# Performance work log

Hardware: AMD Instinct MI355X
Metric: run time of the kernel (lower is better)

The kernel has to match this reference:

```python
import jax, jax.numpy as jnp
import numpy as np

HIDDEN = 1024
HEADS = 16
HEAD_DIM = HIDDEN // HEADS


def setup_inputs() -> dict:
    key = jax.random.key(0)
    ks = jax.random.split(key, 11)
    B, S = 2, 2048
    s = 1.0 / np.sqrt(HIDDEN)
    return {
        "query": jax.random.normal(ks[0], (B, S, HIDDEN), jnp.float32),
        "key": jax.random.normal(ks[1], (B, S, HIDDEN), jnp.float32),
        "value": jax.random.normal(ks[2], (B, S, HIDDEN), jnp.float32),
        "Wq": jax.random.uniform(ks[3], (HIDDEN, HIDDEN), jnp.float32, -s, s),
        "bq": jax.random.uniform(ks[4], (HIDDEN,), jnp.float32, -s, s),
        "Wk": jax.random.uniform(ks[5], (HIDDEN, HIDDEN), jnp.float32, -s, s),
        "bk": jax.random.uniform(ks[6], (HIDDEN,), jnp.float32, -s, s),
        "Wv": jax.random.uniform(ks[7], (HIDDEN, HIDDEN), jnp.float32, -s, s),
        "bv": jax.random.uniform(ks[8], (HIDDEN,), jnp.float32, -s, s),
        "Wo": jax.random.uniform(ks[9], (HIDDEN, HIDDEN), jnp.float32, -s, s),
        "bo": jax.random.uniform(ks[10], (HIDDEN,), jnp.float32, -s, s),
    }


def reference(query, key, value, Wq, bq, Wk, bk, Wv, bv, Wo, bo):
    B, Sq, _ = query.shape
    Sk = key.shape[1]
    # projections (torch Linear: x @ W^T + b)
    Q = (query @ Wq.T + bq).reshape(B, Sq, HEADS, HEAD_DIM).transpose(0, 2, 1, 3)
    K = (key @ Wk.T + bk).reshape(B, Sk, HEADS, HEAD_DIM).transpose(0, 2, 1, 3)
    V = (value @ Wv.T + bv).reshape(B, Sk, HEADS, HEAD_DIM).transpose(0, 2, 1, 3)
    scale = jnp.sqrt(jnp.float32(HEAD_DIM))
    scores = jnp.einsum("bhqd,bhkd->bhqk", Q, K) / scale  # [B,H,Sq,Sk]
    # causal mask (is_causal=True, Sq>1)
    causal = jnp.tril(jnp.ones((Sq, Sk), dtype=bool))
    scores = jnp.where(causal[None, None], scores, -jnp.inf)
    attn = jax.nn.softmax(scores, axis=-1)
    out = jnp.einsum("bhqk,bhkd->bhqd", attn, V)
    out = out.transpose(0, 2, 1, 3).reshape(B, Sq, HIDDEN)
    return out @ Wo.T + bo
```

## Files before the change

### kernel.cpp

```cpp
#include <hip/hip_runtime.h>
#include <hip/hip_bf16.h>


typedef __attribute__((ext_vector_type(4))) float f32x4;
typedef __attribute__((ext_vector_type(8))) short bf16x8;
typedef unsigned short u16;

#define SEQ   2048
#define NH    16
#define HD    64
#define HID   1024
#define CEXP  0.1803368801f
#define MEG   1048576u

#define BAR()  __builtin_amdgcn_s_barrier()
#define SCHED0() __builtin_amdgcn_sched_barrier(0)

static __device__ __forceinline__ u16 f2bf(float f) {
  union { __hip_bfloat16 h; u16 u; } c;
  c.h = __float2bfloat16(f);
  return c.u;
}

static __device__ __forceinline__ int swz(int row, int col8) {
  return col8 ^ ((row & 7) << 3);
}

static __device__ __forceinline__ void gll16(const void* g, void* l) {
  __builtin_amdgcn_global_load_lds(
      (const __attribute__((address_space(1))) void*)g,
      (__attribute__((address_space(3))) void*)l, 16, 0, 0);
}

__global__ __launch_bounds__(256) void cvt_kernel(
    const float* __restrict__ Wq, const float* __restrict__ Wk,
    const float* __restrict__ Wv, const float* __restrict__ Wo,
    const float* __restrict__ q, const float* __restrict__ k,
    const float* __restrict__ v,
    u16* __restrict__ wsout, u16* __restrict__ dob) {
  const int y = blockIdx.y;
  const int c = y & 3;
  const float* src;
  u16* dst;
  if (y < 4) {
    src = (y == 0) ? Wq : (y == 1) ? Wk : (y == 2) ? Wv : Wo;
    dst = wsout + (size_t)y * MEG;
  } else if (y < 8) {
    src = q + (size_t)c * MEG;
    dst = wsout + 4u * MEG + (size_t)c * MEG;
  } else if (y < 12) {
    src = k + (size_t)c * MEG;
    dst = dob + (size_t)c * MEG;
  } else {
    src = v + (size_t)c * MEG;
    dst = dob + 4u * MEG + (size_t)c * MEG;
  }
  int i = (blockIdx.x * 256 + threadIdx.x) * 4;
  float4 f = *(const float4*)(src + i);
  ushort4 o;
  o.x = f2bf(f.x); o.y = f2bf(f.y); o.z = f2bf(f.z); o.w = f2bf(f.w);
  *(ushort4*)(dst + i) = o;
}

__global__ __launch_bounds__(256) void proj_kernel(
    const u16* __restrict__ Xq, const u16* __restrict__ Xk,
    const u16* __restrict__ Xv, const u16* __restrict__ Wc,
    const float* __restrict__ bq, const float* __restrict__ bk,
    const float* __restrict__ bvp,
    u16* __restrict__ Qo, u16* __restrict__ Ko, u16* __restrict__ Vto) {
  __shared__ u16 As[2][128 * 64];
  __shared__ u16 Bs[2][128 * 64];

  const int tid  = threadIdx.x;
  const int lane = tid & 63;
  const int wid  = tid >> 6;
  const int wm   = wid >> 1, wn = wid & 1;
  const int l15  = lane & 15;
  const int lhi  = lane >> 4;
  const int z    = blockIdx.z;
  const int bm   = blockIdx.x * 128;
  const int bn   = blockIdx.y * 128;

  const u16* X = (z == 0) ? Xq : (z == 1) ? Xk : Xv;
  const u16* W = Wc + (size_t)z * (HID * HID);
  const float* bias = (z == 0) ? bq : (z == 1) ? bk : bvp;

  f32x4 acc[4][4];
#pragma unroll
  for (int i = 0; i < 4; i++)
#pragma unroll
    for (int j = 0; j < 4; j++) acc[i][j] = (f32x4){0.f, 0.f, 0.f, 0.f};

  const int lrow  = lane >> 3;
  const int gcol8 = lane & 7;

#define PROJ_STAGE(buf, k0)                                                       \
  {                                                                               \
    _Pragma("unroll")                                                             \
    for (int c = 0; c < 4; c++) {                                                 \
      const int row  = c * 32 + wid * 8 + lrow;                                   \
      const int scol = (gcol8 ^ (row & 7)) * 8;      \
      gll16(X + (size_t)(bm + row) * HID + (k0) + scol,                           \
            (char*)&As[buf][0] + c * 4096 + wid * 1024);                          \
      gll16(W + (size_t)(bn + row) * HID + (k0) + scol,                           \
            (char*)&Bs[buf][0] + c * 4096 + wid * 1024);                          \
    }                                                                             \
  }

  PROJ_STAGE(0, 0);
  for (int t = 0; t < 16; t++) {
    BAR();
    if (t < 15) {
      PROJ_STAGE((t + 1) & 1, (t + 1) * 64);
      asm volatile("s_waitcnt vmcnt(8)" ::: "memory");
    } else {
      asm volatile("s_waitcnt vmcnt(0)" ::: "memory");
    }
    BAR();
    SCHED0();
    const u16* A = &As[t & 1][0];
    const u16* B = &Bs[t & 1][0];
#pragma unroll
    for (int ks = 0; ks < 2; ks++) {
      bf16x8 af[4], bfm[4];
#pragma unroll
      for (int i = 0; i < 4; i++) {
        const int row = wm * 64 + i * 16 + l15;
        af[i] = *(const bf16x8*)&A[row * 64 + swz(row, ks * 32 + lhi * 8)];
      }
#pragma unroll
      for (int j = 0; j < 4; j++) {
        const int row = wn * 64 + j * 16 + l15;
        bfm[j] = *(const bf16x8*)&B[row * 64 + swz(row, ks * 32 + lhi * 8)];
      }
#pragma unroll
      for (int i = 0; i < 4; i++)
#pragma unroll
        for (int j = 0; j < 4; j++)
          acc[i][j] = __builtin_amdgcn_mfma_f32_16x16x32_bf16(af[i], bfm[j], acc[i][j], 0, 0, 0);
    }
  }
#undef PROJ_STAGE

  const int bb = bm >> 11;
#pragma unroll
  for (int j = 0; j < 4; j++) {
    const int n = bn + wn * 64 + j * 16 + l15;
    const float bv_ = bias[n];
    const int h = n >> 6, d = n & 63;
    if (z == 2) {
#pragma unroll
      for (int i = 0; i < 4; i++) {
        const int s0 = (bm + wm * 64 + i * 16 + lhi * 4) & 2047;
        ushort4 t;
        t.x = f2bf(acc[i][j][0] + bv_);
        t.y = f2bf(acc[i][j][1] + bv_);
        t.z = f2bf(acc[i][j][2] + bv_);
        t.w = f2bf(acc[i][j][3] + bv_);
        *(ushort4*)&Vto[((size_t)(bb * NH + h) * HD + d) * SEQ + s0] = t;
      }
    } else {
      u16* O = z ? Ko : Qo;
#pragma unroll
      for (int i = 0; i < 4; i++)
#pragma unroll
        for (int r = 0; r < 4; r++) {
          const int m = bm + wm * 64 + i * 16 + lhi * 4 + r;
          const int s = m & 2047;
          O[(((size_t)(bb * NH + h) * SEQ + s) << 6) + d] = f2bf(acc[i][j][r] + bv_);
        }
    }
  }
}

__global__ __launch_bounds__(512) void attn_kernel(
    const u16* __restrict__ Q, const u16* __restrict__ K,
    const u16* __restrict__ Vt, u16* __restrict__ Aout) {
  __shared__ __align__(16) char pool[51200];

  const int tid  = threadIdx.x;
  const int lane = tid & 63;
  const int wid  = tid >> 6;
  const int rw   = wid & 3;
  const int g    = wid >> 2;
  const int l15  = lane & 15;
  const int lhi  = lane >> 4;

  const int flat = blockIdx.x;
  const int slot = flat >> 3;
  const int bh   = (flat & 7) * 4 + (slot & 3);
  const int qt   = 31 - (slot >> 2);
  const int b    = bh >> 4, h = bh & 15;
  const size_t base = (size_t)bh * SEQ * HD;

  u16* Ksh = (u16*)(pool + g * 8192);
  u16* Vsh = (u16*)(pool + 16384 + g * 8192);
  u16* Psh = (u16*)(pool + 32768 + wid * 2304);

  const int qrow = qt * 64 + rw * 16 + l15;
  bf16x8 aq[2];
  aq[0] = *(const bf16x8*)&Q[base + (size_t)qrow * HD + lhi * 8];
  aq[1] = *(const bf16x8*)&Q[base + (size_t)qrow * HD + 32 + lhi * 8];

  f32x4 o[4];
#pragma unroll
  for (int n = 0; n < 4; n++) o[n] = (f32x4){0.f, 0.f, 0.f, 0.f};
  float m_s = -1e30f, l_s = 0.f;

  const int gt   = tid & 255;
  const int srow = gt >> 2;
  const int sd   = (gt & 3) * 16;

  bf16x8 pk0, pk1, pv0, pv1;

#define ATTN_LOAD(kt_)                                                            \
  {                                                                               \
    const u16* kp = K + base + (size_t)((kt_) * 64 + srow) * HD + sd;             \
    pk0 = *(const bf16x8*)kp;                                                     \
    pk1 = *(const bf16x8*)(kp + 8);                                               \
    const u16* vp = Vt + base + (size_t)srow * SEQ + (kt_) * 64 + sd;             \
    pv0 = *(const bf16x8*)vp;                                                     \
    pv1 = *(const bf16x8*)(vp + 8);                                               \
  }

  if (g <= qt) ATTN_LOAD(g);

  const int nsteps = qt / 2 + 1;
  for (int it = 0; it < nsteps; ++it) {
    const int kt = 2 * it + g;
    const bool act = (kt <= qt);
    BAR();
    if (act) {
      *(bf16x8*)&Ksh[srow * 64 + swz(srow, sd)]     = pk0;
      *(bf16x8*)&Ksh[srow * 64 + swz(srow, sd + 8)] = pk1;
      *(bf16x8*)&Vsh[srow * 64 + swz(srow, sd)]     = pv0;
      *(bf16x8*)&Vsh[srow * 64 + swz(srow, sd + 8)] = pv1;
    }
    const int ktn = kt + 2;
    if (ktn <= qt) ATTN_LOAD(ktn);
    asm volatile("s_waitcnt lgkmcnt(0)" ::: "memory");
    BAR();
    SCHED0();
    if (act) {
      f32x4 sc[4];
      __builtin_amdgcn_s_setprio(1);
#pragma unroll
      for (int n = 0; n < 4; n++) {
        sc[n] = (f32x4){0.f, 0.f, 0.f, 0.f};
#pragma unroll
        for (int ks = 0; ks < 2; ks++) {
          const int krow = n * 16 + l15;
          bf16x8 bk = *(const bf16x8*)&Ksh[krow * 64 + swz(krow, ks * 32 + lhi * 8)];
          sc[n] = __builtin_amdgcn_mfma_f32_16x16x32_bf16(bk, aq[ks], sc[n], 0, 0, 0);
        }
      }
      __builtin_amdgcn_s_setprio(0);
      if (kt == qt) {
#pragma unroll
        for (int n = 0; n < 4; n++)
#pragma unroll
          for (int r = 0; r < 4; r++)
            if (kt * 64 + n * 16 + lhi * 4 + r > qrow) sc[n][r] = -1e30f;
      }
      float mx = -1e30f;
#pragma unroll
      for (int n = 0; n < 4; n++)
        mx = fmaxf(mx, fmaxf(fmaxf(sc[n][0], sc[n][1]), fmaxf(sc[n][2], sc[n][3])));
      mx = fmaxf(mx, __shfl_xor(mx, 16, 64));
      mx = fmaxf(mx, __shfl_xor(mx, 32, 64));
      if (__any(mx > m_s + 64.0f)) {
        const float mnew = fmaxf(m_s, mx);
        const float fac = __builtin_amdgcn_exp2f((m_s - mnew) * CEXP);
        l_s *= fac;
        m_s = mnew;
        float facr[4];
#pragma unroll
        for (int r = 0; r < 4; r++) facr[r] = __shfl(fac, lhi * 4 + r, 64);
#pragma unroll
        for (int n = 0; n < 4; n++) {
          o[n][0] *= facr[0]; o[n][1] *= facr[1];
          o[n][2] *= facr[2]; o[n][3] *= facr[3];
        }
      }
      const float nmc = -m_s * CEXP;
      float ps = 0.f;
      u16 pb[4][4];
#pragma unroll
      for (int n = 0; n < 4; n++)
#pragma unroll
        for (int r = 0; r < 4; r++) {
          const float e = __builtin_amdgcn_exp2f(fmaf(sc[n][r], CEXP, nmc));
          ps += e;
          pb[n][r] = f2bf(e);
        }
      ps += __shfl_xor(ps, 16, 64);
      ps += __shfl_xor(ps, 32, 64);
      l_s += ps;
#pragma unroll
      for (int n = 0; n < 4; n++) {
        ushort4 t; t.x = pb[n][0]; t.y = pb[n][1]; t.z = pb[n][2]; t.w = pb[n][3];
        *(ushort4*)&Psh[l15 * 72 + n * 16 + lhi * 4] = t;
      }
      bf16x8 ap0 = *(const bf16x8*)&Psh[l15 * 72 + lhi * 8];
      bf16x8 ap1 = *(const bf16x8*)&Psh[l15 * 72 + 32 + lhi * 8];
      __builtin_amdgcn_s_setprio(1);
#pragma unroll
      for (int n = 0; n < 4; n++) {
        const int vrow = n * 16 + l15;
        bf16x8 bv0 = *(const bf16x8*)&Vsh[vrow * 64 + swz(vrow, lhi * 8)];
        bf16x8 bv1 = *(const bf16x8*)&Vsh[vrow * 64 + swz(vrow, 32 + lhi * 8)];
        o[n] = __builtin_amdgcn_mfma_f32_16x16x32_bf16(ap0, bv0, o[n], 0, 0, 0);
        o[n] = __builtin_amdgcn_mfma_f32_16x16x32_bf16(ap1, bv1, o[n], 0, 0, 0);
      }
      __builtin_amdgcn_s_setprio(0);
    }
  }
#undef ATTN_LOAD

  __syncthreads();
  float m_o[4], l_o[4];
#pragma unroll
  for (int r = 0; r < 4; r++) {
    m_o[r] = __shfl(m_s, lhi * 4 + r, 64);
    l_o[r] = __shfl(l_s, lhi * 4 + r, 64);
  }

  f32x4* comb = (f32x4*)pool;
  const int ci = (rw * 64 + lane) * 6;
  if (g == 0) {
#pragma unroll
    for (int n = 0; n < 4; n++) comb[ci + n] = o[n];
    comb[ci + 4] = (f32x4){m_o[0], m_o[1], m_o[2], m_o[3]};
    comb[ci + 5] = (f32x4){l_o[0], l_o[1], l_o[2], l_o[3]};
  }
  __syncthreads();
  if (g == 1) {
    f32x4 m0 = comb[ci + 4];
    f32x4 l0 = comb[ci + 5];
    float a0[4], a1[4], inv[4];
#pragma unroll
    for (int r = 0; r < 4; r++) {
      const float m = fmaxf(m0[r], m_o[r]);
      a0[r] = __builtin_amdgcn_exp2f((m0[r] - m) * CEXP);
      a1[r] = __builtin_amdgcn_exp2f((m_o[r] - m) * CEXP);
      inv[r] = 1.0f / (l0[r] * a0[r] + l_o[r] * a1[r]);
    }
#pragma unroll
    for (int n = 0; n < 4; n++) {
      f32x4 o0 = comb[ci + n];
#pragma unroll
      for (int r = 0; r < 4; r++) {
        const int rowg = qt * 64 + rw * 16 + lhi * 4 + r;
        const float val = (o0[r] * a0[r] + o[n][r] * a1[r]) * inv[r];
        Aout[(((size_t)(b * SEQ + rowg)) << 10) + h * 64 + n * 16 + l15] = f2bf(val);
      }
    }
  }
}

__global__ __launch_bounds__(256) void oproj_kernel(
    const u16* __restrict__ X, const u16* __restrict__ W,
    const float* __restrict__ bias, float* __restrict__ Out) {
  __shared__ u16 As[2][128 * 64];
  __shared__ u16 Bs[2][64 * 64];

  const int tid  = threadIdx.x;
  const int lane = tid & 63;
  const int wid  = tid >> 6;
  const int wm   = wid >> 1, wn = wid & 1;
  const int l15  = lane & 15;
  const int lhi  = lane >> 4;
  const int bm   = blockIdx.x * 128;
  const int bn   = blockIdx.y * 64;

  f32x4 acc[4][2];
#pragma unroll
  for (int i = 0; i < 4; i++)
#pragma unroll
    for (int j = 0; j < 2; j++) acc[i][j] = (f32x4){0.f, 0.f, 0.f, 0.f};

  const int lrow  = lane >> 3;
  const int gcol8 = lane & 7;

#define OPROJ_STAGE(buf, k0)                                                      \
  {                                                                               \
    _Pragma("unroll")                                                             \
    for (int c = 0; c < 4; c++) {                                                 \
      const int row  = c * 32 + wid * 8 + lrow;                                   \
      const int scol = (gcol8 ^ (row & 7)) * 8;                                   \
      gll16(X + (size_t)(bm + row) * HID + (k0) + scol,                           \
            (char*)&As[buf][0] + c * 4096 + wid * 1024);                          \
      if (c < 2)                                                                  \
        gll16(W + (size_t)(bn + row) * HID + (k0) + scol,                         \
              (char*)&Bs[buf][0] + c * 4096 + wid * 1024);                        \
    }                                                                             \
  }

  OPROJ_STAGE(0, 0);
  for (int t = 0; t < 16; t++) {
    BAR();
    if (t < 15) {
      OPROJ_STAGE((t + 1) & 1, (t + 1) * 64);
      asm volatile("s_waitcnt vmcnt(6)" ::: "memory");
    } else {
      asm volatile("s_waitcnt vmcnt(0)" ::: "memory");
    }
    BAR();
    SCHED0();
    const u16* A = &As[t & 1][0];
    const u16* B = &Bs[t & 1][0];
#pragma unroll
    for (int ks = 0; ks < 2; ks++) {
      bf16x8 af[4], bfm[2];
#pragma unroll
      for (int i = 0; i < 4; i++) {
        const int row = wm * 64 + i * 16 + l15;
        af[i] = *(const bf16x8*)&A[row * 64 + swz(row, ks * 32 + lhi * 8)];
      }
#pragma unroll
      for (int j = 0; j < 2; j++) {
        const int row = wn * 32 + j * 16 + l15;
        bfm[j] = *(const bf16x8*)&B[row * 64 + swz(row, ks * 32 + lhi * 8)];
      }
#pragma unroll
      for (int i = 0; i < 4; i++)
#pragma unroll
        for (int j = 0; j < 2; j++)
          acc[i][j] = __builtin_amdgcn_mfma_f32_16x16x32_bf16(af[i], bfm[j], acc[i][j], 0, 0, 0);
    }
  }
#undef OPROJ_STAGE

#pragma unroll
  for (int j = 0; j < 2; j++) {
    const int n = bn + wn * 32 + j * 16 + l15;
    const float bv_ = bias[n];
#pragma unroll
    for (int i = 0; i < 4; i++)
#pragma unroll
      for (int r = 0; r < 4; r++) {
        const int m = bm + wm * 64 + i * 16 + lhi * 4 + r;
        Out[(size_t)m * HID + n] = acc[i][j][r] + bv_;
      }
  }
}

extern "C" void kernel_launch(void* const* d_in, const int* in_sizes, int n_in,
                              void* d_out, int out_size, void* d_ws, size_t ws_size,
                              hipStream_t stream) {
  const float* q  = (const float*)d_in[0];
  const float* k  = (const float*)d_in[1];
  const float* v  = (const float*)d_in[2];
  const float* Wq = (const float*)d_in[3];
  const float* bq = (const float*)d_in[4];
  const float* Wk = (const float*)d_in[5];
  const float* bk = (const float*)d_in[6];
  const float* Wv = (const float*)d_in[7];
  const float* bv = (const float*)d_in[8];
  const float* Wo = (const float*)d_in[9];
  const float* bo = (const float*)d_in[10];

  u16* ws   = (u16*)d_ws;
  u16* wqkv = ws;
  u16* wob  = ws + 3u * MEG;
  u16* qb   = ws + 4u * MEG;
  u16* Qb   = ws + 8u * MEG;
  u16* Kb   = ws + 12u * MEG;
  u16* Vtb  = ws + 16u * MEG;
  u16* Ab   = qb;
  u16* kbf  = (u16*)d_out;
  u16* vbf  = (u16*)d_out + 4u * MEG;

  cvt_kernel<<<dim3(1024, 16), 256, 0, stream>>>(Wq, Wk, Wv, Wo, q, k, v, ws, kbf);

  proj_kernel<<<dim3(32, 8, 3), 256, 0, stream>>>(qb, kbf, vbf, wqkv, bq, bk, bv,
                                                  Qb, Kb, Vtb);

  attn_kernel<<<dim3(1024), 512, 0, stream>>>(Qb, Kb, Vtb, Ab);

  oproj_kernel<<<dim3(32, 16), 256, 0, stream>>>(Ab, wob, bo, (float*)d_out);
}
```

Measured before the change: 112.8 us.

## Use 128-row query tiles per block with eight waves sharing each KV tile

The attention kernel used to split each 64-row query tile's KV range across two wave groups and merge the partial softmax results through shared memory. It now gives each block 128 query rows, one 16-row slice per wave, and all eight waves walk every KV tile together. Grid size halves, the cross-group combine and its extra syncthreads disappear, and each KV tile is loaded once per 128 query rows, which halves K/V traffic and shared-memory size. The cost is fewer blocks in flight, causal masking on the last two KV tiles, and longer serial KV loops per block, which can lengthen the tail.

After: 115.3 us. +2.2%, slower.

```diff
diff --git a/kernel.cpp b/kernel.cpp
--- a/kernel.cpp
+++ b/kernel.cpp
@@ -176,28 +176,26 @@
 __global__ __launch_bounds__(512) void attn_kernel(
     const u16* __restrict__ Q, const u16* __restrict__ K,
     const u16* __restrict__ Vt, u16* __restrict__ Aout) {
-  __shared__ __align__(16) char pool[51200];
+  __shared__ __align__(16) char pool[34816];
 
   const int tid  = threadIdx.x;
   const int lane = tid & 63;
   const int wid  = tid >> 6;
-  const int rw   = wid & 3;
-  const int g    = wid >> 2;
   const int l15  = lane & 15;
   const int lhi  = lane >> 4;
 
   const int flat = blockIdx.x;
   const int slot = flat >> 3;
   const int bh   = (flat & 7) * 4 + (slot & 3);
-  const int qt   = 31 - (slot >> 2);
+  const int qt   = 15 - (slot >> 2);
   const int b    = bh >> 4, h = bh & 15;
   const size_t base = (size_t)bh * SEQ * HD;
 
-  u16* Ksh = (u16*)(pool + g * 8192);
-  u16* Vsh = (u16*)(pool + 16384 + g * 8192);
-  u16* Psh = (u16*)(pool + 32768 + wid * 2304);
-
-  const int qrow = qt * 64 + rw * 16 + l15;
+  u16* Ksh = (u16*)(pool);
+  u16* Vsh = (u16*)(pool + 8192);
+  u16* Psh = (u16*)(pool + 16384 + wid * 2304);
+
+  const int qrow = qt * 128 + wid * 16 + l15;
   bf16x8 aq[2];
   aq[0] = *(const bf16x8*)&Q[base + (size_t)qrow * HD + lhi * 8];
   aq[1] = *(const bf16x8*)&Q[base + (size_t)qrow * HD + 32 + lhi * 8];
@@ -207,41 +205,29 @@
   for (int n = 0; n < 4; n++) o[n] = (f32x4){0.f, 0.f, 0.f, 0.f};
   float m_s = -1e30f, l_s = 0.f;
 
-  const int gt   = tid & 255;
-  const int srow = gt >> 2;
-  const int sd   = (gt & 3) * 16;
-
-  bf16x8 pk0, pk1, pv0, pv1;
+  const int srow = tid >> 3;
+  const int sd   = (tid & 7) * 8;
+
+  bf16x8 pk, pv;
 
 #define ATTN_LOAD(kt_)                                                            \
   {                                                                               \
-    const u16* kp = K + base + (size_t)((kt_) * 64 + srow) * HD + sd;             \
-    pk0 = *(const bf16x8*)kp;                                                     \
-    pk1 = *(const bf16x8*)(kp + 8);                                               \
-    const u16* vp = Vt + base + (size_t)srow * SEQ + (kt_) * 64 + sd;             \
-    pv0 = *(const bf16x8*)vp;                                                     \
-    pv1 = *(const bf16x8*)(vp + 8);                                               \
-  }
-
-  if (g <= qt) ATTN_LOAD(g);
-
-  const int nsteps = qt / 2 + 1;
-  for (int it = 0; it < nsteps; ++it) {
-    const int kt = 2 * it + g;
-    const bool act = (kt <= qt);
-    BAR();
-    if (act) {
-      *(bf16x8*)&Ksh[srow * 64 + swz(srow, sd)]     = pk0;
-      *(bf16x8*)&Ksh[srow * 64 + swz(srow, sd + 8)] = pk1;
-      *(bf16x8*)&Vsh[srow * 64 + swz(srow, sd)]     = pv0;
-      *(bf16x8*)&Vsh[srow * 64 + swz(srow, sd + 8)] = pv1;
-    }
-    const int ktn = kt + 2;
-    if (ktn <= qt) ATTN_LOAD(ktn);
+    pk = *(const bf16x8*)&K[base + (size_t)((kt_) * 64 + srow) * HD + sd];        \
+    pv = *(const bf16x8*)&Vt[base + (size_t)srow * SEQ + (kt_) * 64 + sd];        \
+  }
+
+  ATTN_LOAD(0);
+
+  const int nkt = 2 * qt + 2;
+  for (int kt = 0; kt < nkt; ++kt) {
+    BAR();
+    *(bf16x8*)&Ksh[srow * 64 + swz(srow, sd)] = pk;
+    *(bf16x8*)&Vsh[srow * 64 + swz(srow, sd)] = pv;
+    if (kt + 1 < nkt) ATTN_LOAD(kt + 1);
     asm volatile("s_waitcnt lgkmcnt(0)" ::: "memory");
     BAR();
     SCHED0();
-    if (act) {
+    {
       f32x4 sc[4];
       __builtin_amdgcn_s_setprio(1);
 #pragma unroll
@@ -255,7 +241,7 @@
         }
       }
       __builtin_amdgcn_s_setprio(0);
-      if (kt == qt) {
+      if (kt >= 2 * qt) {
 #pragma unroll
         for (int n = 0; n < 4; n++)
 #pragma unroll
@@ -317,43 +303,16 @@
   }
 #undef ATTN_LOAD
 
-  __syncthreads();
-  float m_o[4], l_o[4];
-#pragma unroll
-  for (int r = 0; r < 4; r++) {
-    m_o[r] = __shfl(m_s, lhi * 4 + r, 64);
-    l_o[r] = __shfl(l_s, lhi * 4 + r, 64);
-  }
-
-  f32x4* comb = (f32x4*)pool;
-  const int ci = (rw * 64 + lane) * 6;
-  if (g == 0) {
-#pragma unroll
-    for (int n = 0; n < 4; n++) comb[ci + n] = o[n];
-    comb[ci + 4] = (f32x4){m_o[0], m_o[1], m_o[2], m_o[3]};
-    comb[ci + 5] = (f32x4){l_o[0], l_o[1], l_o[2], l_o[3]};
-  }
-  __syncthreads();
-  if (g == 1) {
-    f32x4 m0 = comb[ci + 4];
-    f32x4 l0 = comb[ci + 5];
-    float a0[4], a1[4], inv[4];
+  float l_o[4];
+#pragma unroll
+  for (int r = 0; r < 4; r++) l_o[r] = __shfl(l_s, lhi * 4 + r, 64);
+#pragma unroll
+  for (int n = 0; n < 4; n++) {
 #pragma unroll
     for (int r = 0; r < 4; r++) {
-      const float m = fmaxf(m0[r], m_o[r]);
-      a0[r] = __builtin_amdgcn_exp2f((m0[r] - m) * CEXP);
-      a1[r] = __builtin_amdgcn_exp2f((m_o[r] - m) * CEXP);
-      inv[r] = 1.0f / (l0[r] * a0[r] + l_o[r] * a1[r]);
-    }
-#pragma unroll
-    for (int n = 0; n < 4; n++) {
-      f32x4 o0 = comb[ci + n];
-#pragma unroll
-      for (int r = 0; r < 4; r++) {
-        const int rowg = qt * 64 + rw * 16 + lhi * 4 + r;
-        const float val = (o0[r] * a0[r] + o[n][r] * a1[r]) * inv[r];
-        Aout[(((size_t)(b * SEQ + rowg)) << 10) + h * 64 + n * 16 + l15] = f2bf(val);
-      }
+      const int rowg = qt * 128 + wid * 16 + lhi * 4 + r;
+      Aout[(((size_t)(b * SEQ + rowg)) << 10) + h * 64 + n * 16 + l15] =
+          f2bf(o[n][r] / l_o[r]);
     }
   }
 }
@@ -476,7 +435,7 @@
   proj_kernel<<<dim3(32, 8, 3), 256, 0, stream>>>(qb, kbf, vbf, wqkv, bq, bk, bv,
                                                   Qb, Kb, Vtb);
 
-  attn_kernel<<<dim3(1024), 512, 0, stream>>>(Qb, Kb, Vtb, Ab);
+  attn_kernel<<<dim3(512), 512, 0, stream>>>(Qb, Kb, Vtb, Ab);
 
   oproj_kernel<<<dim3(32, 16), 256, 0, stream>>>(Ab, wob, bo, (float*)d_out);
 }
```
